# Kernel tuning notes

Measured on AMD Instinct MI355X. Metric: run time of the kernel, lower is better.

Reference implementation:

```python
import jax, jax.numpy as jnp
import numpy as np

ALPHA = 0.2          # LeakyReLU negative slope
NEG_INF = -9e15      # mask value used by the torch module


def setup_inputs() -> dict:
    key = jax.random.key(0)
    k_x, k_adj, k_w, k_a = jax.random.split(key, 4)
    B, N, D, L = 8, 2048, 128, 3
    x = jax.random.normal(k_x, (B, N, D), dtype=jnp.float32)
    adj = jax.random.randint(k_adj, (B, N, N), 0, 2, dtype=jnp.int32)
    Wg = jax.random.normal(k_w, (L, D, D), dtype=jnp.float32) * 0.08  # ~Linear init scale
    bg = jnp.zeros((L, D), dtype=jnp.float32)
    attn_a = jax.random.normal(k_a, (L, 2 * D), dtype=jnp.float32) * 0.08
    return {"x": x, "adj": adj, "Wg": Wg, "bg": bg, "attn_a": attn_a}


def reference(x, adj, Wg, bg, attn_a):
    # x: [B,N,D], adj: [B,N,N] int, Wg: [L,D,D], bg: [L,D], attn_a: [L,2D]
    D = x.shape[-1]
    L = Wg.shape[0]
    mask = adj > 0
    for i in range(L):  # small fixed layer loop
        h = jax.nn.relu(x @ Wg[i] + bg[i])                       # [B,N,D]
        # a_input[b,i,j] = [h_i, h_j]; dot with a splits into two rank-1 terms,
        # avoiding the N*N*2D intermediate while computing identical math.
        s1 = h @ attn_a[i, :D]                                   # [B,N]
        s2 = h @ attn_a[i, D:]                                   # [B,N]
        e = jax.nn.leaky_relu(s1[:, :, None] + s2[:, None, :], ALPHA)  # [B,N,N]
        e = jnp.where(mask, e, NEG_INF)
        attn = jax.nn.softmax(e, axis=2)                         # masked softmax over neighbors
        # dropout p=0.0 -> identity
        x = x + jnp.einsum('bij,bjd->bid', attn, h)              # residual update
    return x
```

## Files before the change

kernel.cpp:

```cpp
#include <hip/hip_runtime.h>
#include <stdint.h>

typedef __attribute__((ext_vector_type(8))) short short8;
typedef __attribute__((ext_vector_type(4))) float f32x4;
typedef __attribute__((ext_vector_type(16))) float f32x16;
typedef __attribute__((ext_vector_type(4))) unsigned uint4v;

__device__ __forceinline__ unsigned short f2bf(float f) {
    unsigned u = __float_as_uint(f);
    unsigned r = u + 0x7fffu + ((u >> 16) & 1u);
    return (unsigned short)(r >> 16);
}
__device__ __forceinline__ unsigned fenc(float f) {
    unsigned u = __float_as_uint(f);
    return (u & 0x80000000u) ? ~u : (u | 0x80000000u);
}
__device__ __forceinline__ float fdec(unsigned e) {
    unsigned u = (e & 0x80000000u) ? (e & 0x7fffffffu) : ~e;
    return __uint_as_float(u);
}

__global__ __launch_bounds__(256) void k_init(const float* __restrict__ xin,
                                              const float* __restrict__ Wf,
                                              float* __restrict__ xq,
                                              unsigned short* __restrict__ wTb,
                                              unsigned* __restrict__ s2mx) {
    int blk = blockIdx.x, tid = threadIdx.x;
    if (blk < 2048) {
        int e0 = (blk * 256 + tid) * 4;
        *(f32x4*)(xq + e0) = *(const f32x4*)(xin + e0);
    } else if (blk < 2240) {
        int c = (blk - 2048) * 256 + tid;
        int l = c >> 14, rem = c & 16383, n = rem >> 7, k = rem & 127;
        wTb[c] = f2bf(Wf[l * 16384 + k * 128 + n]);
    } else if (tid < 24) {
        s2mx[tid] = fenc(-3e38f);
    }
}

__global__ __launch_bounds__(256) void k_pack(const int* __restrict__ adj,
                                              unsigned long long* __restrict__ packed) {
    int w = (blockIdx.x * 256 + threadIdx.x) >> 6;
    int lane = threadIdx.x & 63;
    for (int k = 0; k < 64; k++) {
        int q = w * 64 + k;
        int row = q >> 5, wd = q & 31;
        int v = adj[row * 2048 + wd * 64 + lane];
        unsigned long long m = __ballot(v > 0);
        if (lane == 0) packed[q] = m;
    }
}

__global__ __launch_bounds__(256) void k_h(
    const float* __restrict__ xq, const unsigned short* __restrict__ wTb,
    const float* __restrict__ bF, const float* __restrict__ aF, int layer,
    unsigned short* __restrict__ hP, float* __restrict__ s1g,
    float* __restrict__ s2g, unsigned* __restrict__ s2mx)
{
    __shared__ short xs[64 * 136];
    __shared__ short wsb[128 * 136];
    __shared__ float s2blk[4];
    int blk = blockIdx.x, tid = threadIdx.x;
    int row0 = blk * 64, b = blk >> 5;
    int w = tid >> 6, lane = tid & 63, quad = lane >> 4, l15 = lane & 15;

    for (int c = tid; c < 1024; c += 256) {
        int r = c >> 4, kg = c & 15;
        const float* src = &xq[(row0 + r) * 128 + kg * 8];
        f32x4 v0 = *(const f32x4*)src;
        f32x4 v1 = *(const f32x4*)(src + 4);
        short8 o;
        o[0] = (short)f2bf(v0[0]); o[1] = (short)f2bf(v0[1]);
        o[2] = (short)f2bf(v0[2]); o[3] = (short)f2bf(v0[3]);
        o[4] = (short)f2bf(v1[0]); o[5] = (short)f2bf(v1[1]);
        o[6] = (short)f2bf(v1[2]); o[7] = (short)f2bf(v1[3]);
        *(short8*)&xs[r * 136 + kg * 8] = o;
    }
    const unsigned short* wl = wTb + layer * 16384;
    for (int c = tid; c < 2048; c += 256) {
        int n = c >> 4, kg = c & 15;
        *(short8*)&wsb[n * 136 + kg * 8] = *(const short8*)&wl[n * 128 + kg * 8];
    }
    __syncthreads();

    f32x4 acc[8];
#pragma unroll
    for (int t = 0; t < 8; t++) acc[t] = {0.f, 0.f, 0.f, 0.f};
#pragma unroll
    for (int ks = 0; ks < 4; ks++) {
        short8 af = *(const short8*)&xs[(w * 16 + l15) * 136 + ks * 32 + quad * 8];
#pragma unroll
        for (int t = 0; t < 8; t++) {
            short8 bf = *(const short8*)&wsb[(t * 16 + l15) * 136 + ks * 32 + quad * 8];
            acc[t] = __builtin_amdgcn_mfma_f32_16x16x32_bf16(af, bf, acc[t], 0, 0, 0);
        }
    }

    float s1p[4] = {0.f, 0.f, 0.f, 0.f}, s2p[4] = {0.f, 0.f, 0.f, 0.f};
#pragma unroll
    for (int t = 0; t < 8; t++) {
        int colg = t * 16 + l15;
        float bgf = bF[layer * 128 + colg];
        float a1 = aF[layer * 256 + colg];
        float a2 = aF[layer * 256 + 128 + colg];
#pragma unroll
        for (int r = 0; r < 4; r++) {
            float v = acc[t][r] + bgf;
            v = v > 0.f ? v : 0.f;
            acc[t][r] = v;
            s1p[r] = fmaf(v, a1, s1p[r]);
            s2p[r] = fmaf(v, a2, s2p[r]);
        }
    }
#pragma unroll
    for (int r = 0; r < 4; r++) {
#pragma unroll
        for (int off = 1; off < 16; off <<= 1) {
            s1p[r] += __shfl_xor(s1p[r], off, 64);
            s2p[r] += __shfl_xor(s2p[r], off, 64);
        }
    }
    if (l15 == 0) {
#pragma unroll
        for (int r = 0; r < 4; r++) {
            int rowg = row0 + w * 16 + quad * 4 + r;
            s1g[rowg] = s1p[r];
            s2g[rowg] = s2p[r];
        }
    }
    float mx = fmaxf(fmaxf(s2p[0], s2p[1]), fmaxf(s2p[2], s2p[3]));
    mx = fmaxf(mx, __shfl_xor(mx, 16, 64));
    mx = fmaxf(mx, __shfl_xor(mx, 32, 64));
    if (lane == 0) s2blk[w] = mx;
    __syncthreads();

    short* st = (short*)wsb;
#pragma unroll
    for (int t = 0; t < 8; t++)
#pragma unroll
        for (int r = 0; r < 4; r++)
            st[(w * 16 + quad * 4 + r) * 130 + t * 16 + l15] = (short)f2bf(acc[t][r]);
    __syncthreads();
    if (tid == 0) {
        float m2 = fmaxf(fmaxf(s2blk[0], s2blk[1]), fmaxf(s2blk[2], s2blk[3]));
        atomicMax(&s2mx[layer * 8 + b], fenc(m2));
    }
    int i0 = (blk & 31) * 64;
    for (int c = tid; c < 1024; c += 256) {
        int t = c >> 8, jl2 = (c >> 6) & 3, sl = c & 63;
        int d = t * 32 + (sl & 31);
        int jloc = jl2 * 16 + (sl >> 5) * 8;
        short8 o;
#pragma unroll
        for (int i = 0; i < 8; i++) o[i] = st[(jloc + i) * 130 + d];
        int jtg = (i0 >> 4) + jl2;
        *(short8*)&hP[(((size_t)(b * 4 + t) * 128 + jtg) * 64 + sl) * 8] = o;
    }
}

__global__ __launch_bounds__(256) void k_attn(
    const unsigned long long* __restrict__ packed,
    const unsigned short* __restrict__ hP, const float* __restrict__ s1g,
    const float* __restrict__ s2g, const unsigned* __restrict__ s2mx,
    int layer, float* __restrict__ Opart, float* __restrict__ Ppart)
{
    int blk = blockIdx.x, tid = threadIdx.x;
    int b = blk >> 6;
    int rowg0 = blk * 32;
    int w = tid >> 6, lane = tid & 63;
    int col = lane & 31, khalf = lane >> 5;

    float s1v = s1g[rowg0 + col];
    float s2m = fdec(s2mx[layer * 8 + b]);
    float tmh = s1v + s2m;
    float mhat = fmaxf(tmh, 0.2f * tmh);

    f32x16 acc[5];
#pragma unroll
    for (int t = 0; t < 5; t++)
#pragma unroll
        for (int r = 0; r < 16; r++) acc[t][r] = 0.f;

    short8 onesf;
    {
        short v = (col == 0) ? (short)0x3F80 : (short)0;
        onesf[0]=v;onesf[1]=v;onesf[2]=v;onesf[3]=v;onesf[4]=v;onesf[5]=v;onesf[6]=v;onesf[7]=v;
    }

    const float* s2b = s2g + b * 2048;
    const unsigned short* hPb = hP + (size_t)b * 4 * 128 * 64 * 8;
    const unsigned long long* prow = packed + (size_t)(rowg0 + col) * 32;

    unsigned long long word = 0;
#pragma unroll 4
    for (int jl = 0; jl < 32; jl++) {
        int jt = w * 32 + jl;
        if ((jl & 3) == 0) word = prow[jt >> 2];
        unsigned b8 = (unsigned)(word >> ((jt & 3) * 16 + khalf * 8)) & 0xffu;
        int j0 = jt * 16 + khalf * 8;
        f32x4 sa = *(const f32x4*)&s2b[j0];
        f32x4 sb = *(const f32x4*)&s2b[j0 + 4];
        float sv[8] = {sa[0], sa[1], sa[2], sa[3], sb[0], sb[1], sb[2], sb[3]};
        unsigned rp[8];
#pragma unroll
        for (int jj = 0; jj < 8; jj++) {
            float e = s1v + sv[jj];
            e = fmaxf(e, 0.2f * e);
            float pv = __expf(e - mhat);
            rp[jj] = (b8 & (1u << jj)) ? (__float_as_uint(pv) + 0x8000u) : 0u;
        }
        uint4v pk;
        pk[0] = (rp[0] >> 16) | (rp[1] & 0xffff0000u);
        pk[1] = (rp[2] >> 16) | (rp[3] & 0xffff0000u);
        pk[2] = (rp[4] >> 16) | (rp[5] & 0xffff0000u);
        pk[3] = (rp[6] >> 16) | (rp[7] & 0xffff0000u);
        short8 af = *(short8*)&pk;
        short8 bfr[4];
#pragma unroll
        for (int t = 0; t < 4; t++)
            bfr[t] = *(const short8*)&hPb[(((size_t)t * 128 + jt) * 64 + lane) * 8];
#pragma unroll
        for (int t = 0; t < 4; t++)
            acc[t] = __builtin_amdgcn_mfma_f32_32x32x16_bf16(af, bfr[t], acc[t], 0, 0, 0);
        acc[4] = __builtin_amdgcn_mfma_f32_32x32x16_bf16(af, onesf, acc[4], 0, 0, 0);
    }

#pragma unroll
    for (int reg = 0; reg < 16; reg++) {
        int row = (reg & 3) + 8 * (reg >> 2) + 4 * khalf;
        int rowgC = rowg0 + row;
#pragma unroll
        for (int t = 0; t < 4; t++)
            Opart[((size_t)w * 16384 + rowgC) * 128 + t * 32 + col] = acc[t][reg];
        if (col == 0) Ppart[w * 16384 + rowgC] = acc[4][reg];
    }
}

__global__ __launch_bounds__(256) void k_comb(
    const float* __restrict__ Opart, const float* __restrict__ Ppart,
    float* __restrict__ xq)
{
    int idx = blockIdx.x * 256 + threadIdx.x;
    int row = idx >> 5;
    float p = Ppart[row] + Ppart[16384 + row] + Ppart[32768 + row] + Ppart[49152 + row];
    float rl = p > 0.f ? 1.0f / p : 0.f;
    f32x4 o0 = *(const f32x4*)&Opart[(size_t)idx * 4];
    f32x4 o1 = *(const f32x4*)&Opart[(size_t)idx * 4 + 2097152];
    f32x4 o2 = *(const f32x4*)&Opart[(size_t)idx * 4 + 4194304];
    f32x4 o3 = *(const f32x4*)&Opart[(size_t)idx * 4 + 6291456];
    f32x4 xv = *(const f32x4*)&xq[idx * 4];
#pragma unroll
    for (int k = 0; k < 4; k++) xv[k] += (o0[k] + o1[k] + o2[k] + o3[k]) * rl;
    *(f32x4*)&xq[idx * 4] = xv;
}

extern "C" void kernel_launch(void* const* d_in, const int* in_sizes, int n_in,
                              void* d_out, int out_size, void* d_ws, size_t ws_size,
                              hipStream_t stream) {
    const void* px = d_in[0];
    int ia = 1; long amax = -1;
    for (int i = 1; i < n_in; i++)
        if ((long)in_sizes[i] > amax) { amax = in_sizes[i]; ia = i; }
    int rem[8]; int m = 0;
    for (int i = 1; i < n_in && m < 8; i++) if (i != ia) rem[m++] = i;
    for (int i = 0; i < m; i++)
        for (int j = i + 1; j < m; j++)
            if (in_sizes[rem[j]] > in_sizes[rem[i]]) { int t = rem[i]; rem[i] = rem[j]; rem[j] = t; }
    const int*   padj = (const int*)((n_in > 1) ? d_in[ia] : d_in[0]);
    const float* pW = (const float*)((m > 0) ? d_in[rem[0]] : d_in[0]);
    const float* pa = (const float*)((m > 1) ? d_in[rem[1]] : d_in[0]);
    const float* pb = (const float*)((m > 2) ? d_in[rem[2]] : d_in[0]);

    float* xq = (float*)d_out;
    char* ws = (char*)d_ws;
    unsigned long long* packed = (unsigned long long*)ws;
    unsigned short* hP = (unsigned short*)(ws + 4194304);
    float* s1 = (float*)(ws + 8388608);
    float* s2 = (float*)(ws + 8454144);
    unsigned* s2mx = (unsigned*)(ws + 8519680);
    unsigned short* wTb = (unsigned short*)(ws + 8519808);
    float* Opart = (float*)(ws + 16777216);
    float* Ppart = (float*)(ws + 50331648);

    k_init<<<2241, 256, 0, stream>>>((const float*)px, pW, xq, wTb, s2mx);
    k_pack<<<2048, 256, 0, stream>>>(padj, packed);
    for (int l = 0; l < 3; l++) {
        k_h<<<256, 256, 0, stream>>>(xq, wTb, pb, pa, l, hP, s1, s2, s2mx);
        k_attn<<<512, 256, 0, stream>>>(packed, hP, s1, s2, s2mx, l, Opart, Ppart);
        k_comb<<<2048, 256, 0, stream>>>(Opart, Ppart, xq);
    }
}
```

Measured before the change: 363.4 us.

## Fuse split-K reduction into attention kernel via shared memory and merge setup kernels

The four per-wave partial outputs of the attention kernel are now reduced in shared memory and added straight into x, which removes the Opart/Ppart global round trip and the separate combine kernel for each layer. The per-wave split of the key tiles changes from contiguous chunks to an interleaved pattern, so each lane loads one packed adjacency word per iteration. The adjacency-pack and init kernels are merged into one launch. This adds about 50KB of shared memory per block, which may lower occupancy, and wave 0 does the final reduction serially.

```diff
diff --git a/kernel.cpp b/kernel.cpp
--- a/kernel.cpp
+++ b/kernel.cpp
@@ -20,34 +20,32 @@
     return __uint_as_float(u);
 }
 
-__global__ __launch_bounds__(256) void k_init(const float* __restrict__ xin,
-                                              const float* __restrict__ Wf,
-                                              float* __restrict__ xq,
-                                              unsigned short* __restrict__ wTb,
-                                              unsigned* __restrict__ s2mx) {
+__global__ __launch_bounds__(256) void k_setup(
+    const float* __restrict__ xin, const float* __restrict__ Wf,
+    const int* __restrict__ adj, float* __restrict__ xq,
+    unsigned short* __restrict__ wTb, unsigned* __restrict__ s2mx,
+    unsigned long long* __restrict__ packed)
+{
     int blk = blockIdx.x, tid = threadIdx.x;
     if (blk < 2048) {
-        int e0 = (blk * 256 + tid) * 4;
+        int w = (blk * 256 + tid) >> 6;
+        int lane = tid & 63;
+        for (int k = 0; k < 64; k++) {
+            int q = w * 64 + k;
+            int row = q >> 5, wd = q & 31;
+            int v = adj[row * 2048 + wd * 64 + lane];
+            unsigned long long m = __ballot(v > 0);
+            if (lane == 0) packed[q] = m;
+        }
+    } else if (blk < 4096) {
+        int e0 = ((blk - 2048) * 256 + tid) * 4;
         *(f32x4*)(xq + e0) = *(const f32x4*)(xin + e0);
-    } else if (blk < 2240) {
-        int c = (blk - 2048) * 256 + tid;
+    } else if (blk < 4288) {
+        int c = (blk - 4096) * 256 + tid;
         int l = c >> 14, rem = c & 16383, n = rem >> 7, k = rem & 127;
         wTb[c] = f2bf(Wf[l * 16384 + k * 128 + n]);
     } else if (tid < 24) {
         s2mx[tid] = fenc(-3e38f);
-    }
-}
-
-__global__ __launch_bounds__(256) void k_pack(const int* __restrict__ adj,
-                                              unsigned long long* __restrict__ packed) {
-    int w = (blockIdx.x * 256 + threadIdx.x) >> 6;
-    int lane = threadIdx.x & 63;
-    for (int k = 0; k < 64; k++) {
-        int q = w * 64 + k;
-        int row = q >> 5, wd = q & 31;
-        int v = adj[row * 2048 + wd * 64 + lane];
-        unsigned long long m = __ballot(v > 0);
-        if (lane == 0) packed[q] = m;
     }
 }
 
@@ -162,8 +160,10 @@
     const unsigned long long* __restrict__ packed,
     const unsigned short* __restrict__ hP, const float* __restrict__ s1g,
     const float* __restrict__ s2g, const unsigned* __restrict__ s2mx,
-    int layer, float* __restrict__ Opart, float* __restrict__ Ppart)
+    int layer, float* __restrict__ xq)
 {
+    __shared__ float red[3 * 32 * 128];
+    __shared__ float red_p[4 * 32];
     int blk = blockIdx.x, tid = threadIdx.x;
     int b = blk >> 6;
     int rowg0 = blk * 32;
@@ -191,12 +191,10 @@
     const unsigned short* hPb = hP + (size_t)b * 4 * 128 * 64 * 8;
     const unsigned long long* prow = packed + (size_t)(rowg0 + col) * 32;
 
-    unsigned long long word = 0;
-#pragma unroll 4
     for (int jl = 0; jl < 32; jl++) {
-        int jt = w * 32 + jl;
-        if ((jl & 3) == 0) word = prow[jt >> 2];
-        unsigned b8 = (unsigned)(word >> ((jt & 3) * 16 + khalf * 8)) & 0xffu;
+        int jt = w + jl * 4;
+        unsigned long long word = prow[jl];
+        unsigned b8 = (unsigned)(word >> (w * 16 + khalf * 8)) & 0xffu;
         int j0 = jt * 16 + khalf * 8;
         f32x4 sa = *(const f32x4*)&s2b[j0];
         f32x4 sb = *(const f32x4*)&s2b[j0 + 4];
@@ -228,30 +226,28 @@
 #pragma unroll
     for (int reg = 0; reg < 16; reg++) {
         int row = (reg & 3) + 8 * (reg >> 2) + 4 * khalf;
-        int rowgC = rowg0 + row;
-#pragma unroll
-        for (int t = 0; t < 4; t++)
-            Opart[((size_t)w * 16384 + rowgC) * 128 + t * 32 + col] = acc[t][reg];
-        if (col == 0) Ppart[w * 16384 + rowgC] = acc[4][reg];
-    }
-}
-
-__global__ __launch_bounds__(256) void k_comb(
-    const float* __restrict__ Opart, const float* __restrict__ Ppart,
-    float* __restrict__ xq)
-{
-    int idx = blockIdx.x * 256 + threadIdx.x;
-    int row = idx >> 5;
-    float p = Ppart[row] + Ppart[16384 + row] + Ppart[32768 + row] + Ppart[49152 + row];
-    float rl = p > 0.f ? 1.0f / p : 0.f;
-    f32x4 o0 = *(const f32x4*)&Opart[(size_t)idx * 4];
-    f32x4 o1 = *(const f32x4*)&Opart[(size_t)idx * 4 + 2097152];
-    f32x4 o2 = *(const f32x4*)&Opart[(size_t)idx * 4 + 4194304];
-    f32x4 o3 = *(const f32x4*)&Opart[(size_t)idx * 4 + 6291456];
-    f32x4 xv = *(const f32x4*)&xq[idx * 4];
-#pragma unroll
-    for (int k = 0; k < 4; k++) xv[k] += (o0[k] + o1[k] + o2[k] + o3[k]) * rl;
-    *(f32x4*)&xq[idx * 4] = xv;
+        if (w > 0) {
+#pragma unroll
+            for (int t = 0; t < 4; t++)
+                red[(w - 1) * 4096 + row * 128 + t * 32 + col] = acc[t][reg];
+        }
+        if (col == 0) red_p[w * 32 + row] = acc[4][reg];
+    }
+    __syncthreads();
+    if (w == 0) {
+#pragma unroll
+        for (int reg = 0; reg < 16; reg++) {
+            int row = (reg & 3) + 8 * (reg >> 2) + 4 * khalf;
+            float p = red_p[row] + red_p[32 + row] + red_p[64 + row] + red_p[96 + row];
+            float rl = p > 0.f ? 1.0f / p : 0.f;
+#pragma unroll
+            for (int t = 0; t < 4; t++) {
+                int cidx = row * 128 + t * 32 + col;
+                float o = acc[t][reg] + red[cidx] + red[4096 + cidx] + red[8192 + cidx];
+                xq[(rowg0 + row) * 128 + t * 32 + col] += o * rl;
+            }
+        }
+    }
 }
 
 extern "C" void kernel_launch(void* const* d_in, const int* in_sizes, int n_in,
@@ -279,14 +275,10 @@
     float* s2 = (float*)(ws + 8454144);
     unsigned* s2mx = (unsigned*)(ws + 8519680);
     unsigned short* wTb = (unsigned short*)(ws + 8519808);
-    float* Opart = (float*)(ws + 16777216);
-    float* Ppart = (float*)(ws + 50331648);
-
-    k_init<<<2241, 256, 0, stream>>>((const float*)px, pW, xq, wTb, s2mx);
-    k_pack<<<2048, 256, 0, stream>>>(padj, packed);
+
+    k_setup<<<4289, 256, 0, stream>>>((const float*)px, pW, padj, xq, wTb, s2mx, packed);
     for (int l = 0; l < 3; l++) {
         k_h<<<256, 256, 0, stream>>>(xq, wTb, pb, pa, l, hP, s1, s2, s2mx);
-        k_attn<<<512, 256, 0, stream>>>(packed, hP, s1, s2, s2mx, l, Opart, Ppart);
-        k_comb<<<2048, 256, 0, stream>>>(Opart, Ppart, xq);
-    }
-}
+        k_attn<<<512, 256, 0, stream>>>(packed, hP, s1, s2, s2mx, l, xq);
+    }
+}
```

Result: faster. 344.7 us (-5.2%).
